# Kernel optimization log

Measured on AMD Instinct MI355X. Metric: run time of the kernel, lower is better.

Reference implementation:

```python
import math
import jax, jax.numpy as jnp
import numpy as np

C = 1.0          # Poincare ball curvature
NUM_HEADS = 8
EPS = 1e-15

def _beta(a, b):
    # Beta function via lgamma (python float constant)
    return math.exp(math.lgamma(a) + math.lgamma(b) - math.lgamma(a + b))

def h_linear(x, z, r, c=C):
    """HNN++ Poincare fully-connected layer (hypll HLinear).
    x: [..., in] points in the ball; z: [in, out] tangent weights; r: [out] bias."""
    sc = math.sqrt(c)
    x2 = jnp.sum(x * x, axis=-1, keepdims=True)
    lam = 2.0 / (1.0 - c * x2)                                # conformal factor
    zn = jnp.maximum(jnp.linalg.norm(z, axis=0), EPS)          # [out]
    inner = x @ z                                              # [..., out]
    two_scr = 2.0 * sc * r
    d = (2.0 * zn / sc) * jnp.arcsinh(
        (sc * inner * lam / zn) * jnp.cosh(two_scr) - (lam - 1.0) * jnp.sinh(two_scr)
    )
    w = jnp.sinh(sc * d) / sc
    return w / (1.0 + jnp.sqrt(1.0 + c * jnp.sum(w * w, axis=-1, keepdims=True)))

def pairwise_dist(q, k, c=C):
    """Poincare distance d(q,k) = arccosh(1 + 2c|q-k|^2 / ((1-c|q|^2)(1-c|k|^2))) / sqrt(c).
    q,k: [B,H,S,hd] -> [B,H,S,S]."""
    q2 = jnp.sum(q * q, axis=-1)
    k2 = jnp.sum(k * k, axis=-1)
    qk = jnp.einsum('bhqd,bhkd->bhqk', q, k)
    diff2 = jnp.maximum(q2[..., :, None] + k2[..., None, :] - 2.0 * qk, 0.0)
    denom = (1.0 - c * q2)[..., :, None] * (1.0 - c * k2)[..., None, :]
    arg = 1.0 + 2.0 * c * diff2 / denom
    return jnp.arccosh(jnp.maximum(arg, 1.0 + 1e-7)) / math.sqrt(c)

def midpoint(v, w, c=C):
    """Weighted Mobius gyromidpoint: m = 1/2 (x) (sum w*lam*x / sum w*(lam-1)).
    v: [B,H,Sk,hd], w: [B,H,Sq,Sk] -> [B,H,Sq,hd]."""
    v2 = jnp.sum(v * v, axis=-1)                      # [B,H,Sk]
    lam = 2.0 / (1.0 - c * v2)
    num = jnp.einsum('bhqk,bhkd->bhqd', w * lam[..., None, :], v)
    den = jnp.maximum(jnp.einsum('bhqk,bhk->bhq', w, lam - 1.0), EPS)[..., None]
    g = num / den                                     # gyromidpoint pre-scaling
    sc = math.sqrt(c)
    gn = jnp.maximum(jnp.linalg.norm(g, axis=-1, keepdims=True), EPS)
    t = jnp.tanh(0.5 * jnp.arctanh(jnp.clip(sc * gn, 0.0, 1.0 - 1e-7)))
    return (t / sc) * g / gn

def _forward(query, key, value, Wq, bq, Wk, bk, Wv, bv, scale_tau, scale_gamma):
    B, S, E = query.shape
    H = NUM_HEADS
    hd = E // H
    # hyperbolic q/k/v projections, then split into heads: [B,H,S,hd]
    q = h_linear(query, Wq, bq).reshape(B, S, H, hd).transpose(0, 2, 1, 3)
    k = h_linear(key, Wk, bk).reshape(B, S, H, hd).transpose(0, 2, 1, 3)
    v = h_linear(value, Wv, bv).reshape(B, S, H, hd).transpose(0, 2, 1, 3)
    # similarity = -dist/tau - gamma with tau = exp(-scale_tau)
    sim = -pairwise_dist(q, k) * jnp.exp(scale_tau[0]) - scale_gamma[0]
    causal = jnp.triu(jnp.ones((S, S), dtype=bool), k=1)
    sim = jnp.where(causal, -jnp.inf, sim)
    w = jnp.exp(sim)                                  # 'exp' attention activation
    agg = midpoint(v, w)                              # [B,H,S,hd]
    agg = agg.transpose(0, 2, 1, 3).reshape(B, S, E)
    # HNN++ beta-concatenation of the per-head ball points
    scale = _beta(E / 2.0, 0.5) / _beta(hd / 2.0, 0.5)
    return agg * scale

def setup_inputs() -> dict:
    root = jax.random.key(0)
    ks = jax.random.split(root, 8)
    B, S, E = 1, 2048, 512
    s = 0.02  # keep points well inside the unit ball
    return {
        'query': s * jax.random.normal(ks[0], (B, S, E), jnp.float32),
        'key':   s * jax.random.normal(ks[1], (B, S, E), jnp.float32),
        'value': s * jax.random.normal(ks[2], (B, S, E), jnp.float32),
        'Wq': s * jax.random.normal(ks[3], (E, E), jnp.float32),
        'Wk': s * jax.random.normal(ks[4], (E, E), jnp.float32),
        'Wv': s * jax.random.normal(ks[5], (E, E), jnp.float32),
        'bq': jnp.zeros((E,), jnp.float32),
        'bk': jnp.zeros((E,), jnp.float32),
        'bv': jnp.zeros((E,), jnp.float32),
        'scale_tau': jnp.zeros((1,), jnp.float32),
        'scale_gamma': jnp.zeros((1,), jnp.float32),
    }

def reference(query, key, value, Wq, Wk, Wv, bq, bk, bv, scale_tau, scale_gamma):
    return _forward(query, key, value, Wq, bq, Wk, bk, Wv, bv, scale_tau, scale_gamma)
```

## Files before the change

kernel.cpp:

```cpp
#include <hip/hip_runtime.h>
#include <cmath>

#define H 8
#define SEQ 2048
#define EDIM 512
#define HD 64
#define EPSF 1e-15f

typedef short bf16x8 __attribute__((ext_vector_type(8)));
typedef float f32x4 __attribute__((ext_vector_type(4)));

#define FLAG_OFF  0
#define ZN_OFF    16
#define X2S_OFF   (ZN_OFF + 3 * EDIM)
#define STATS_OFF (X2S_OFF + 3 * SEQ)
#define CQ_OFF    (STATS_OFF + 3 * H * SEQ)
#define IK_OFF    (CQ_OFF + H * SEQ)
#define U16_OFF   (IK_OFF + H * SEQ + 16)
#define WT_U16    0
#define XB_U16    (WT_U16 + 3 * EDIM * EDIM)
#define QKVB_U16  (XB_U16 + 3 * SEQ * EDIM)
#define VT_U16    (QKVB_U16 + 3 * SEQ * EDIM)
#define U16_TOTAL (VT_U16 + H * 80 * SEQ)
#define PART_OFF  (U16_OFF + (U16_TOTAL + 1) / 2 + 16)

__device__ __forceinline__ float bf2f(unsigned short u){
  union { unsigned int i; float f; } v; v.i = ((unsigned int)u) << 16; return v.f;
}
__device__ __forceinline__ unsigned short f2bf(float f){
  union { float f; unsigned int i; } v; v.f = f;
  unsigned int x = v.i;
  unsigned int r = (x + 0x7fffu + ((x >> 16) & 1u)) >> 16;
  return (unsigned short)r;
}

__global__ void probe_kernel(const unsigned short* __restrict__ q, int* __restrict__ flag){
  const int t = threadIdx.x;
  float mx = 0.f;
  #pragma unroll
  for (int j = 0; j < 4; ++j) mx = fmaxf(mx, fabsf(bf2f(q[t * 4 + j])));
  #pragma unroll
  for (int m = 32; m >= 1; m >>= 1) mx = fmaxf(mx, __shfl_xor(mx, m, 64));
  if (t == 0) *flag = (mx > 1000.f) ? 1 : 0;
}

__global__ __launch_bounds__(256) void wcvt_kernel(
    const void* __restrict__ Wq, const void* __restrict__ Wk, const void* __restrict__ Wv,
    const int* __restrict__ flag, unsigned short* __restrict__ WT, float* __restrict__ zn)
{
  const int p = blockIdx.y;
  const int bi = blockIdx.x >> 3, bo = blockIdx.x & 7;
  const void* W = (p == 0) ? Wq : ((p == 1) ? Wk : Wv);
  const int t = threadIdx.x;
  const int isf32 = *flag;
  __shared__ float tile[64][65];

  #pragma unroll
  for (int j = 0; j < 16; ++j){
    int idx = t + 256 * j;
    int il = idx >> 6, ol = idx & 63;
    float val;
    if (isf32) val = ((const float*)W)[(size_t)(bi * 64 + il) * EDIM + bo * 64 + ol];
    else       val = bf2f(((const unsigned short*)W)[(size_t)(bi * 64 + il) * EDIM + bo * 64 + ol]);
    tile[il][ol] = val;
  }
  __syncthreads();
  if (t < 64){
    float s = 0.f;
    #pragma unroll 8
    for (int i = 0; i < 64; ++i){ float v = tile[i][t]; s += v * v; }
    atomicAdd(&zn[p * EDIM + bo * 64 + t], s);
  }
  #pragma unroll
  for (int j = 0; j < 16; ++j){
    int idx = t + 256 * j;
    int ol = idx >> 6, il = idx & 63;
    WT[((size_t)p * EDIM + bo * 64 + ol) * EDIM + bi * 64 + il] = f2bf(tile[il][ol]);
  }
}

__global__ __launch_bounds__(256) void xcvt_kernel(
    const void* __restrict__ Xq, const void* __restrict__ Xk, const void* __restrict__ Xv,
    const int* __restrict__ flag, unsigned short* __restrict__ Xb, float* __restrict__ x2s)
{
  const int p = blockIdx.y;
  const void* X = (p == 0) ? Xq : ((p == 1) ? Xk : Xv);
  const int row = blockIdx.x * 8 + (threadIdx.x >> 5);
  const int l = threadIdx.x & 31;
  const int isf32 = *flag;
  float s = 0.f;
  #pragma unroll
  for (int j = 0; j < 16; ++j){
    int i = l + 32 * j;
    float val;
    if (isf32) val = ((const float*)X)[(size_t)row * EDIM + i];
    else       val = bf2f(((const unsigned short*)X)[(size_t)row * EDIM + i]);
    Xb[((size_t)p * SEQ + row) * EDIM + i] = f2bf(val);
    s += val * val;
  }
  #pragma unroll
  for (int m = 16; m >= 1; m >>= 1) s += __shfl_xor(s, m, 64);
  if (l == 0) x2s[p * SEQ + row] = s;
}

__global__ __launch_bounds__(256) void hlinear_kernel(
    const unsigned short* __restrict__ Xb, const unsigned short* __restrict__ WT,
    const void* __restrict__ Bq, const void* __restrict__ Bk, const void* __restrict__ Bv,
    const float* __restrict__ znacc, const float* __restrict__ x2s_g,
    const int* __restrict__ flag,
    unsigned short* __restrict__ qkvb, float* __restrict__ stats,
    float* __restrict__ cqs, float* __restrict__ iks,
    unsigned short* __restrict__ VT)
{
  const int p = blockIdx.y;
  const void* Bb = (p == 0) ? Bq : ((p == 1) ? Bk : Bv);
  const int r0 = blockIdx.x * 8;
  const int t  = threadIdx.x;
  const int w = t >> 6, lane = t & 63;
  const int col = lane & 15, quad = lane >> 4;
  const int isf32 = *flag;

  __shared__ float smem[8 * EDIM];
  __shared__ float sw2[8];

  const unsigned short* Xrow = Xb + ((size_t)p * SEQ + r0 + (col & 7)) * EDIM;
  const unsigned short* WTb  = WT + ((size_t)p * EDIM + w * 128 + col) * EDIM;

  f32x4 acc[8];
  #pragma unroll
  for (int nt = 0; nt < 8; ++nt) acc[nt] = (f32x4){0.f, 0.f, 0.f, 0.f};

  for (int ks = 0; ks < 16; ++ks){
    bf16x8 af = *(const bf16x8*)&Xrow[ks * 32 + quad * 8];
    #pragma unroll
    for (int nt = 0; nt < 8; ++nt){
      bf16x8 bf = *(const bf16x8*)&WTb[(size_t)nt * 16 * EDIM + ks * 32 + quad * 8];
      acc[nt] = __builtin_amdgcn_mfma_f32_16x16x32_bf16(af, bf, acc[nt], 0, 0, 0);
    }
  }

  if (quad < 2){
    float lamr[4], lm1[4];
    #pragma unroll
    for (int r = 0; r < 4; ++r){
      float x2 = x2s_g[p * SEQ + r0 + quad * 4 + r];
      lamr[r] = 2.f / (1.f - x2);
      lm1[r] = lamr[r] - 1.f;
    }
    #pragma unroll
    for (int nt = 0; nt < 8; ++nt){
      const int n = w * 128 + nt * 16 + col;
      float znv = fmaxf(sqrtf(znacc[p * EDIM + n]), EPSF);
      float rb;
      if (isf32) rb = ((const float*)Bb)[n];
      else       rb = bf2f(((const unsigned short*)Bb)[n]);
      float e2r = __expf(2.f * rb);
      float ie2r = 1.f / e2r;
      float ch = 0.5f * (e2r + ie2r), sh = 0.5f * (e2r - ie2r);
      float izn = 1.f / znv;
      float tz = 2.f * znv;
      #pragma unroll
      for (int r = 0; r < 4; ++r){
        float a = (acc[nt][r] * lamr[r] * izn) * ch - lm1[r] * sh;
        float b = a + sqrtf(a * a + 1.f);
        float tt = __expf(tz * __logf(b));
        smem[(quad * 4 + r) * EDIM + n] = 0.5f * (tt - 1.f / tt);
      }
    }
  }
  __syncthreads();

  {
    int row = t >> 5, l = t & 31;
    float s = 0.f;
    for (int o = l; o < EDIM; o += 32){ float wv = smem[row * EDIM + o]; s += wv * wv; }
    #pragma unroll
    for (int m = 16; m >= 1; m >>= 1) s += __shfl_xor(s, m, 64);
    if (l == 0) sw2[row] = s;
  }
  __syncthreads();

  const int o0 = 2 * t;
  const int h0 = t >> 5;
  const int d0 = o0 & 63;
  #pragma unroll
  for (int rr = 0; rr < 8; ++rr){
    float inv = 1.f / (1.f + sqrtf(1.f + sw2[rr]));
    unsigned short b0 = f2bf(smem[rr * EDIM + o0] * inv);
    unsigned short b1 = f2bf(smem[rr * EDIM + o0 + 1] * inv);
    float r0v = bf2f(b0), r1v = bf2f(b1);
    int s = r0 + rr;
    unsigned int* dst = (unsigned int*)&qkvb[(((size_t)p * H + h0) * SEQ + s) * HD + d0];
    *dst = (unsigned int)b0 | ((unsigned int)b1 << 16);
    float ss = r0v * r0v + r1v * r1v;
    #pragma unroll
    for (int m = 16; m >= 1; m >>= 1) ss += __shfl_xor(ss, m, 64);
    if (p == 2){
      float lam = 2.f / (1.f - ss);
      VT[((size_t)h0 * 80 + d0) * SEQ + s]     = f2bf(r0v * lam);
      VT[((size_t)h0 * 80 + d0 + 1) * SEQ + s] = f2bf(r1v * lam);
      if ((t & 31) == 0) VT[((size_t)h0 * 80 + 64) * SEQ + s] = f2bf(lam - 1.f);
    }
    if ((t & 31) == 0){
      stats[((size_t)p * H + h0) * SEQ + s] = ss;
      if (p == 0) cqs[(size_t)h0 * SEQ + s] = 2.f / (1.f - ss);
      if (p == 1) iks[(size_t)h0 * SEQ + s] = 1.f / (1.f - ss);
    }
  }
}

__global__ __launch_bounds__(256) void attn_part_kernel(
    const unsigned short* __restrict__ Qb, const unsigned short* __restrict__ Kb,
    const unsigned short* __restrict__ VT,
    const float* __restrict__ q2s_all, const float* __restrict__ k2s_all,
    const float* __restrict__ cqs_all, const float* __restrict__ iks_all,
    const void* __restrict__ tau, const void* __restrict__ gam,
    const int* __restrict__ flag, float4* __restrict__ part)
{
  const int h  = blockIdx.y;
  const int tile = blockIdx.x >> 1;
  const int sl = blockIdx.x & 1;
  const int t = threadIdx.x;
  const int w = t >> 6, lane = t & 63;
  const int col = lane & 15, quad = lane >> 4;
  const int q0 = tile * 16;

  const unsigned short* Qh  = Qb + (size_t)h * SEQ * HD;
  const unsigned short* Kh  = Kb + (size_t)h * SEQ * HD;
  const unsigned short* VTh = VT + (size_t)h * 80 * SEQ;
  const float* q2s = q2s_all + (size_t)h * SEQ;
  const float* k2s = k2s_all + (size_t)h * SEQ;
  const float* cqs = cqs_all + (size_t)h * SEQ;
  const float* iks = iks_all + (size_t)h * SEQ;

  __shared__ float red[4][64][20];

  float tauv, gamv;
  if (*flag){ tauv = ((const float*)tau)[0]; gamv = ((const float*)gam)[0]; }
  else      { tauv = bf2f(((const unsigned short*)tau)[0]);
              gamv = bf2f(((const unsigned short*)gam)[0]); }
  const float e_tau = expf(tauv);

  const int srcA = ((quad & 1) * 2) * 16 + col;
  const int srcB = srcA + 16;
  const int tsel = quad >> 1;

  bf16x8 qf0 = *(const bf16x8*)&Qh[(size_t)(q0 + col) * HD + quad * 8];
  bf16x8 qf1 = *(const bf16x8*)&Qh[(size_t)(q0 + col) * HD + 32 + quad * 8];
  const float q2 = q2s[q0 + col];
  const float cq = cqs[q0 + col];
  const int qmax = q0 + col;

  f32x4 pv[5];
  #pragma unroll
  for (int nt = 0; nt < 5; ++nt) pv[nt] = (f32x4){0.f, 0.f, 0.f, 0.f};

  const int nch = (tile + 4) >> 2;
  for (int kc = sl * 4 + w; kc < nch; kc += 8){
    #pragma unroll
    for (int half = 0; half < 2; ++half){
      const int kb32 = kc * 64 + half * 32;
      unsigned int tlo[2], thi[2];
      #pragma unroll
      for (int tt = 0; tt < 2; ++tt){
        const int kbase = kb32 + 16 * tt;
        bf16x8 kf0 = *(const bf16x8*)&Kh[(size_t)(kbase + col) * HD + quad * 8];
        bf16x8 kf1 = *(const bf16x8*)&Kh[(size_t)(kbase + col) * HD + 32 + quad * 8];
        f32x4 s = (f32x4){0.f, 0.f, 0.f, 0.f};
        s = __builtin_amdgcn_mfma_f32_16x16x32_bf16(kf0, qf0, s, 0, 0, 0);
        s = __builtin_amdgcn_mfma_f32_16x16x32_bf16(kf1, qf1, s, 0, 0, 0);
        float4 k2q = *(const float4*)&k2s[kbase + quad * 4];
        float4 ikq = *(const float4*)&iks[kbase + quad * 4];
        unsigned short pb[4];
        #pragma unroll
        for (int r = 0; r < 4; ++r){
          float k2 = (r == 0) ? k2q.x : (r == 1) ? k2q.y : (r == 2) ? k2q.z : k2q.w;
          float ik = (r == 0) ? ikq.x : (r == 1) ? ikq.y : (r == 2) ? ikq.z : ikq.w;
          float diff2 = fmaxf(q2 + k2 - 2.f * s[r], 0.f);
          float u = diff2 * cq * ik;
          u = fmaxf(u, 1e-7f);
          float z = 1.f + u + sqrtf(u * (u + 2.f));
          float wv = __expf(-e_tau * __logf(z) - gamv);
          int key = kbase + quad * 4 + r;
          if (key > qmax) wv = 0.f;
          pb[r] = f2bf(wv);
        }
        tlo[tt] = (unsigned int)pb[0] | ((unsigned int)pb[1] << 16);
        thi[tt] = (unsigned int)pb[2] | ((unsigned int)pb[3] << 16);
      }
      unsigned int a0 = (unsigned int)__shfl((int)tlo[0], srcA, 64);
      unsigned int a1 = (unsigned int)__shfl((int)tlo[1], srcA, 64);
      unsigned int b0 = (unsigned int)__shfl((int)thi[0], srcA, 64);
      unsigned int b1 = (unsigned int)__shfl((int)thi[1], srcA, 64);
      unsigned int c0 = (unsigned int)__shfl((int)tlo[0], srcB, 64);
      unsigned int c1 = (unsigned int)__shfl((int)tlo[1], srcB, 64);
      unsigned int d0 = (unsigned int)__shfl((int)thi[0], srcB, 64);
      unsigned int d1 = (unsigned int)__shfl((int)thi[1], srcB, 64);
      union { uint4 u; bf16x8 v; } pw;
      pw.u.x = tsel ? a1 : a0;
      pw.u.y = tsel ? b1 : b0;
      pw.u.z = tsel ? c1 : c0;
      pw.u.w = tsel ? d1 : d0;
      #pragma unroll
      for (int nt = 0; nt < 5; ++nt){
        bf16x8 vf = *(const bf16x8*)&VTh[(size_t)(16 * nt + col) * SEQ + kb32 + quad * 8];
        pv[nt] = __builtin_amdgcn_mfma_f32_16x16x32_bf16(pw.v, vf, pv[nt], 0, 0, 0);
      }
    }
  }

  #pragma unroll
  for (int nt = 0; nt < 5; ++nt)
    *(float4*)&red[w][lane][nt * 4] = (float4){pv[nt][0], pv[nt][1], pv[nt][2], pv[nt][3]};
  __syncthreads();

  if (t < 64){
    const size_t base = (((size_t)h * 128 + tile) * 2 + sl) * 5;
    #pragma unroll
    for (int nt = 0; nt < 5; ++nt){
      float4 a = *(const float4*)&red[0][t][nt * 4];
      float4 b = *(const float4*)&red[1][t][nt * 4];
      float4 c = *(const float4*)&red[2][t][nt * 4];
      float4 d = *(const float4*)&red[3][t][nt * 4];
      part[(base + nt) * 64 + t] =
          (float4){a.x + b.x + c.x + d.x, a.y + b.y + c.y + d.y,
                   a.z + b.z + c.z + d.z, a.w + b.w + c.w + d.w};
    }
  }
}

__global__ __launch_bounds__(64) void attn_fin_kernel(
    const float4* __restrict__ part, float* __restrict__ out, float beta_scale)
{
  const int h = blockIdx.y, tile = blockIdx.x;
  const int t = threadIdx.x;
  const int col = t & 15, quad = t >> 4;
  const int q0 = tile * 16;

  f32x4 pv[5];
  const size_t b0 = (((size_t)h * 128 + tile) * 2 + 0) * 5;
  const size_t b1 = (((size_t)h * 128 + tile) * 2 + 1) * 5;
  #pragma unroll
  for (int nt = 0; nt < 5; ++nt){
    float4 a = part[(b0 + nt) * 64 + t];
    float4 b = part[(b1 + nt) * 64 + t];
    pv[nt] = (f32x4){a.x + b.x, a.y + b.y, a.z + b.z, a.w + b.w};
  }

  #pragma unroll
  for (int r = 0; r < 4; ++r){
    float den = __shfl(pv[4][r], quad * 16, 64);
    den = fmaxf(den, EPSF);
    float inv_den = 1.f / den;
    float g[4];
    float gsq = 0.f;
    #pragma unroll
    for (int nt = 0; nt < 4; ++nt){ g[nt] = pv[nt][r] * inv_den; gsq += g[nt] * g[nt]; }
    #pragma unroll
    for (int m = 8; m >= 1; m >>= 1) gsq += __shfl_xor(gsq, m, 64);
    float gn = fmaxf(sqrtf(gsq), EPSF);
    float x = fminf(gn, 1.f - 1e-7f);
    float tt2 = x / (1.f + sqrtf(1.f - x * x));
    float scl = (tt2 / gn) * beta_scale;
    const int q = q0 + quad * 4 + r;
    #pragma unroll
    for (int nt = 0; nt < 4; ++nt)
      out[(size_t)q * EDIM + h * HD + 16 * nt + col] = g[nt] * scl;
  }
}

extern "C" void kernel_launch(void* const* d_in, const int* in_sizes, int n_in,
                              void* d_out, int out_size, void* d_ws, size_t ws_size,
                              hipStream_t stream){
  const void* Xq  = d_in[0];
  const void* Xk  = d_in[1];
  const void* Xv  = d_in[2];
  const void* Wq  = d_in[3];
  const void* Wk  = d_in[4];
  const void* Wv  = d_in[5];
  const void* Bq  = d_in[6];
  const void* Bk  = d_in[7];
  const void* Bv  = d_in[8];
  const void* tau = d_in[9];
  const void* gam = d_in[10];

  float* wsf   = (float*)d_ws;
  int*   flag  = (int*)(wsf + FLAG_OFF);
  float* zn    = wsf + ZN_OFF;
  float* x2s   = wsf + X2S_OFF;
  float* stats = wsf + STATS_OFF;
  float* cqs   = wsf + CQ_OFF;
  float* iks   = wsf + IK_OFF;
  unsigned short* u16b = (unsigned short*)(wsf + U16_OFF);
  unsigned short* WT   = u16b + WT_U16;
  unsigned short* Xb   = u16b + XB_U16;
  unsigned short* qkvb = u16b + QKVB_U16;
  unsigned short* VT   = u16b + VT_U16;
  float4* part = (float4*)(wsf + PART_OFF);

  unsigned short* Qb = qkvb;
  unsigned short* Kb = qkvb + (size_t)H * SEQ * HD;
  float* q2s = stats;
  float* k2s = stats + (size_t)H * SEQ;

  double lb1 = lgamma(EDIM / 2.0) + lgamma(0.5) - lgamma(EDIM / 2.0 + 0.5);
  double lb2 = lgamma(HD / 2.0)   + lgamma(0.5) - lgamma(HD / 2.0 + 0.5);
  float beta_scale = (float)exp(lb1 - lb2);

  probe_kernel<<<dim3(1), dim3(64), 0, stream>>>((const unsigned short*)Xq, flag);
  hipMemsetAsync(zn, 0, 3 * EDIM * sizeof(float), stream);
  hipMemsetAsync(VT, 0, (size_t)H * 80 * SEQ * sizeof(unsigned short), stream);
  wcvt_kernel<<<dim3(64, 3), dim3(256), 0, stream>>>(Wq, Wk, Wv, flag, WT, zn);
  xcvt_kernel<<<dim3(SEQ / 8, 3), dim3(256), 0, stream>>>(Xq, Xk, Xv, flag, Xb, x2s);
  hlinear_kernel<<<dim3(SEQ / 8, 3), dim3(256), 0, stream>>>(
      Xb, WT, Bq, Bk, Bv, zn, x2s, flag, qkvb, stats, cqs, iks, VT);
  attn_part_kernel<<<dim3(256, H), dim3(256), 0, stream>>>(
      Qb, Kb, VT, q2s, k2s, cqs, iks, tau, gam, flag, part);
  attn_fin_kernel<<<dim3(128, H), dim3(64), 0, stream>>>(
      part, (float*)d_out, beta_scale);
}
```

Measured before the change: 231.6 us.

## Fuse input conversion into HLinear and use atomic split-K attention accumulation

Removes the separate input-conversion kernel: the HLinear GEMM now reads raw inputs, converts them to bf16 and computes row norms in-register, and handles 16 rows per block so no MFMA rows are wasted. The attention kernel is restructured so each block covers 64 queries (one per wave) and splits the causal key chunks across 8 slices, with early exit for empty slices. Partial results go into a zeroed fp32 accumulator through atomics, replacing the shared-memory reduction and partial buffer. In exchange it adds atomic traffic, a larger memset, and a summation order that is no longer deterministic.

```diff
diff --git a/kernel.cpp b/kernel.cpp
--- a/kernel.cpp
+++ b/kernel.cpp
@@ -12,17 +12,14 @@
 
 #define FLAG_OFF  0
 #define ZN_OFF    16
-#define X2S_OFF   (ZN_OFF + 3 * EDIM)
-#define STATS_OFF (X2S_OFF + 3 * SEQ)
+#define ACC_OFF   (ZN_OFF + 3 * EDIM)
+#define STATS_OFF (ACC_OFF + H * SEQ * 80)
 #define CQ_OFF    (STATS_OFF + 3 * H * SEQ)
 #define IK_OFF    (CQ_OFF + H * SEQ)
 #define U16_OFF   (IK_OFF + H * SEQ + 16)
 #define WT_U16    0
-#define XB_U16    (WT_U16 + 3 * EDIM * EDIM)
-#define QKVB_U16  (XB_U16 + 3 * SEQ * EDIM)
+#define QKVB_U16  (WT_U16 + 3 * EDIM * EDIM)
 #define VT_U16    (QKVB_U16 + 3 * SEQ * EDIM)
-#define U16_TOTAL (VT_U16 + H * 80 * SEQ)
-#define PART_OFF  (U16_OFF + (U16_TOTAL + 1) / 2 + 16)
 
 __device__ __forceinline__ float bf2f(unsigned short u){
   union { unsigned int i; float f; } v; v.i = ((unsigned int)u) << 16; return v.f;
@@ -79,103 +76,92 @@
   }
 }
 
-__global__ __launch_bounds__(256) void xcvt_kernel(
+__global__ __launch_bounds__(256) void hlinear_kernel(
     const void* __restrict__ Xq, const void* __restrict__ Xk, const void* __restrict__ Xv,
-    const int* __restrict__ flag, unsigned short* __restrict__ Xb, float* __restrict__ x2s)
-{
-  const int p = blockIdx.y;
-  const void* X = (p == 0) ? Xq : ((p == 1) ? Xk : Xv);
-  const int row = blockIdx.x * 8 + (threadIdx.x >> 5);
-  const int l = threadIdx.x & 31;
-  const int isf32 = *flag;
-  float s = 0.f;
-  #pragma unroll
-  for (int j = 0; j < 16; ++j){
-    int i = l + 32 * j;
-    float val;
-    if (isf32) val = ((const float*)X)[(size_t)row * EDIM + i];
-    else       val = bf2f(((const unsigned short*)X)[(size_t)row * EDIM + i]);
-    Xb[((size_t)p * SEQ + row) * EDIM + i] = f2bf(val);
-    s += val * val;
-  }
-  #pragma unroll
-  for (int m = 16; m >= 1; m >>= 1) s += __shfl_xor(s, m, 64);
-  if (l == 0) x2s[p * SEQ + row] = s;
-}
-
-__global__ __launch_bounds__(256) void hlinear_kernel(
-    const unsigned short* __restrict__ Xb, const unsigned short* __restrict__ WT,
+    const unsigned short* __restrict__ WT,
     const void* __restrict__ Bq, const void* __restrict__ Bk, const void* __restrict__ Bv,
-    const float* __restrict__ znacc, const float* __restrict__ x2s_g,
-    const int* __restrict__ flag,
+    const float* __restrict__ znacc, const int* __restrict__ flag,
     unsigned short* __restrict__ qkvb, float* __restrict__ stats,
     float* __restrict__ cqs, float* __restrict__ iks,
     unsigned short* __restrict__ VT)
 {
   const int p = blockIdx.y;
+  const void* X  = (p == 0) ? Xq : ((p == 1) ? Xk : Xv);
   const void* Bb = (p == 0) ? Bq : ((p == 1) ? Bk : Bv);
-  const int r0 = blockIdx.x * 8;
+  const int r0 = blockIdx.x * 16;
   const int t  = threadIdx.x;
   const int w = t >> 6, lane = t & 63;
   const int col = lane & 15, quad = lane >> 4;
   const int isf32 = *flag;
 
-  __shared__ float smem[8 * EDIM];
-  __shared__ float sw2[8];
-
-  const unsigned short* Xrow = Xb + ((size_t)p * SEQ + r0 + (col & 7)) * EDIM;
-  const unsigned short* WTb  = WT + ((size_t)p * EDIM + w * 128 + col) * EDIM;
+  __shared__ float smem[16 * EDIM];
+  __shared__ float sw2[16];
+
+  const unsigned short* WTb = WT + ((size_t)p * EDIM + w * 128 + col) * EDIM;
+  const float* Xf = (const float*)X + (size_t)(r0 + col) * EDIM;
+  const unsigned short* Xh = (const unsigned short*)X + (size_t)(r0 + col) * EDIM;
 
   f32x4 acc[8];
   #pragma unroll
   for (int nt = 0; nt < 8; ++nt) acc[nt] = (f32x4){0.f, 0.f, 0.f, 0.f};
+  float x2part = 0.f;
 
   for (int ks = 0; ks < 16; ++ks){
-    bf16x8 af = *(const bf16x8*)&Xrow[ks * 32 + quad * 8];
+    bf16x8 af;
+    if (isf32){
+      float4 xa = *(const float4*)&Xf[ks * 32 + quad * 8];
+      float4 xb = *(const float4*)&Xf[ks * 32 + quad * 8 + 4];
+      float xv[8] = {xa.x, xa.y, xa.z, xa.w, xb.x, xb.y, xb.z, xb.w};
+      #pragma unroll
+      for (int j = 0; j < 8; ++j){ af[j] = (short)f2bf(xv[j]); x2part += xv[j] * xv[j]; }
+    } else {
+      af = *(const bf16x8*)&Xh[ks * 32 + quad * 8];
+      #pragma unroll
+      for (int j = 0; j < 8; ++j){ float xv = bf2f((unsigned short)af[j]); x2part += xv * xv; }
+    }
     #pragma unroll
     for (int nt = 0; nt < 8; ++nt){
       bf16x8 bf = *(const bf16x8*)&WTb[(size_t)nt * 16 * EDIM + ks * 32 + quad * 8];
       acc[nt] = __builtin_amdgcn_mfma_f32_16x16x32_bf16(af, bf, acc[nt], 0, 0, 0);
     }
   }
-
-  if (quad < 2){
-    float lamr[4], lm1[4];
+  x2part += __shfl_xor(x2part, 16, 64);
+  x2part += __shfl_xor(x2part, 32, 64);
+  float lamr[4], lm1[4];
+  #pragma unroll
+  for (int r = 0; r < 4; ++r){
+    float x2r = __shfl(x2part, quad * 4 + r, 64);
+    lamr[r] = 2.f / (1.f - x2r);
+    lm1[r] = lamr[r] - 1.f;
+  }
+  #pragma unroll
+  for (int nt = 0; nt < 8; ++nt){
+    const int n = w * 128 + nt * 16 + col;
+    float znv = fmaxf(sqrtf(znacc[p * EDIM + n]), EPSF);
+    float rb;
+    if (isf32) rb = ((const float*)Bb)[n];
+    else       rb = bf2f(((const unsigned short*)Bb)[n]);
+    float e2r = __expf(2.f * rb);
+    float ie2r = 1.f / e2r;
+    float ch = 0.5f * (e2r + ie2r), sh = 0.5f * (e2r - ie2r);
+    float izn = 1.f / znv;
+    float tz = 2.f * znv;
     #pragma unroll
     for (int r = 0; r < 4; ++r){
-      float x2 = x2s_g[p * SEQ + r0 + quad * 4 + r];
-      lamr[r] = 2.f / (1.f - x2);
-      lm1[r] = lamr[r] - 1.f;
-    }
-    #pragma unroll
-    for (int nt = 0; nt < 8; ++nt){
-      const int n = w * 128 + nt * 16 + col;
-      float znv = fmaxf(sqrtf(znacc[p * EDIM + n]), EPSF);
-      float rb;
-      if (isf32) rb = ((const float*)Bb)[n];
-      else       rb = bf2f(((const unsigned short*)Bb)[n]);
-      float e2r = __expf(2.f * rb);
-      float ie2r = 1.f / e2r;
-      float ch = 0.5f * (e2r + ie2r), sh = 0.5f * (e2r - ie2r);
-      float izn = 1.f / znv;
-      float tz = 2.f * znv;
-      #pragma unroll
-      for (int r = 0; r < 4; ++r){
-        float a = (acc[nt][r] * lamr[r] * izn) * ch - lm1[r] * sh;
-        float b = a + sqrtf(a * a + 1.f);
-        float tt = __expf(tz * __logf(b));
-        smem[(quad * 4 + r) * EDIM + n] = 0.5f * (tt - 1.f / tt);
-      }
+      float a = (acc[nt][r] * lamr[r] * izn) * ch - lm1[r] * sh;
+      float b = a + sqrtf(a * a + 1.f);
+      float tt = __expf(tz * __logf(b));
+      smem[(quad * 4 + r) * EDIM + n] = 0.5f * (tt - 1.f / tt);
     }
   }
   __syncthreads();
 
   {
-    int row = t >> 5, l = t & 31;
+    int row = t >> 4, l = t & 15;
     float s = 0.f;
-    for (int o = l; o < EDIM; o += 32){ float wv = smem[row * EDIM + o]; s += wv * wv; }
-    #pragma unroll
-    for (int m = 16; m >= 1; m >>= 1) s += __shfl_xor(s, m, 64);
+    for (int o = l; o < EDIM; o += 16){ float wv = smem[row * EDIM + o]; s += wv * wv; }
+    #pragma unroll
+    for (int m = 8; m >= 1; m >>= 1) s += __shfl_xor(s, m, 16);
     if (l == 0) sw2[row] = s;
   }
   __syncthreads();
@@ -183,8 +169,9 @@
   const int o0 = 2 * t;
   const int h0 = t >> 5;
   const int d0 = o0 & 63;
-  #pragma unroll
-  for (int rr = 0; rr < 8; ++rr){
+  const int l5 = t & 31;
+  #pragma unroll
+  for (int rr = 0; rr < 16; ++rr){
     float inv = 1.f / (1.f + sqrtf(1.f + sw2[rr]));
     unsigned short b0 = f2bf(smem[rr * EDIM + o0] * inv);
     unsigned short b1 = f2bf(smem[rr * EDIM + o0 + 1] * inv);
@@ -199,9 +186,10 @@
       float lam = 2.f / (1.f - ss);
       VT[((size_t)h0 * 80 + d0) * SEQ + s]     = f2bf(r0v * lam);
       VT[((size_t)h0 * 80 + d0 + 1) * SEQ + s] = f2bf(r1v * lam);
-      if ((t & 31) == 0) VT[((size_t)h0 * 80 + 64) * SEQ + s] = f2bf(lam - 1.f);
-    }
-    if ((t & 31) == 0){
+      if (l5 < 16)
+        VT[((size_t)h0 * 80 + 64 + l5) * SEQ + s] = (l5 == 0) ? f2bf(lam - 1.f) : 0;
+    }
+    if (l5 == 0){
       stats[((size_t)p * H + h0) * SEQ + s] = ss;
       if (p == 0) cqs[(size_t)h0 * SEQ + s] = 2.f / (1.f - ss);
       if (p == 1) iks[(size_t)h0 * SEQ + s] = 1.f / (1.f - ss);
@@ -209,21 +197,22 @@
   }
 }
 
-__global__ __launch_bounds__(256) void attn_part_kernel(
+__global__ __launch_bounds__(256) void attn_kernel(
     const unsigned short* __restrict__ Qb, const unsigned short* __restrict__ Kb,
     const unsigned short* __restrict__ VT,
     const float* __restrict__ q2s_all, const float* __restrict__ k2s_all,
     const float* __restrict__ cqs_all, const float* __restrict__ iks_all,
     const void* __restrict__ tau, const void* __restrict__ gam,
-    const int* __restrict__ flag, float4* __restrict__ part)
+    const int* __restrict__ flag, float* __restrict__ ACC)
 {
   const int h  = blockIdx.y;
-  const int tile = blockIdx.x >> 1;
-  const int sl = blockIdx.x & 1;
+  const int tile = blockIdx.x >> 3;
+  const int sl = blockIdx.x & 7;
+  if (sl > tile) return;
   const int t = threadIdx.x;
   const int w = t >> 6, lane = t & 63;
   const int col = lane & 15, quad = lane >> 4;
-  const int q0 = tile * 16;
+  const int q0 = tile * 64 + w * 16;
 
   const unsigned short* Qh  = Qb + (size_t)h * SEQ * HD;
   const unsigned short* Kh  = Kb + (size_t)h * SEQ * HD;
@@ -233,8 +222,6 @@
   const float* cqs = cqs_all + (size_t)h * SEQ;
   const float* iks = iks_all + (size_t)h * SEQ;
 
-  __shared__ float red[4][64][20];
-
   float tauv, gamv;
   if (*flag){ tauv = ((const float*)tau)[0]; gamv = ((const float*)gam)[0]; }
   else      { tauv = bf2f(((const unsigned short*)tau)[0]);
@@ -255,8 +242,7 @@
   #pragma unroll
   for (int nt = 0; nt < 5; ++nt) pv[nt] = (f32x4){0.f, 0.f, 0.f, 0.f};
 
-  const int nch = (tile + 4) >> 2;
-  for (int kc = sl * 4 + w; kc < nch; kc += 8){
+  for (int kc = sl; kc <= tile; kc += 8){
     #pragma unroll
     for (int half = 0; half < 2; ++half){
       const int kb32 = kc * 64 + half * 32;
@@ -277,8 +263,7 @@
           float k2 = (r == 0) ? k2q.x : (r == 1) ? k2q.y : (r == 2) ? k2q.z : k2q.w;
           float ik = (r == 0) ? ikq.x : (r == 1) ? ikq.y : (r == 2) ? ikq.z : ikq.w;
           float diff2 = fmaxf(q2 + k2 - 2.f * s[r], 0.f);
-          float u = diff2 * cq * ik;
-          u = fmaxf(u, 1e-7f);
+          float u = fmaxf(diff2 * cq * ik, 1e-7f);
           float z = 1.f + u + sqrtf(u * (u + 2.f));
           float wv = __expf(-e_tau * __logf(z) - gamv);
           int key = kbase + quad * 4 + r;
@@ -310,27 +295,16 @@
   }
 
   #pragma unroll
-  for (int nt = 0; nt < 5; ++nt)
-    *(float4*)&red[w][lane][nt * 4] = (float4){pv[nt][0], pv[nt][1], pv[nt][2], pv[nt][3]};
-  __syncthreads();
-
-  if (t < 64){
-    const size_t base = (((size_t)h * 128 + tile) * 2 + sl) * 5;
-    #pragma unroll
-    for (int nt = 0; nt < 5; ++nt){
-      float4 a = *(const float4*)&red[0][t][nt * 4];
-      float4 b = *(const float4*)&red[1][t][nt * 4];
-      float4 c = *(const float4*)&red[2][t][nt * 4];
-      float4 d = *(const float4*)&red[3][t][nt * 4];
-      part[(base + nt) * 64 + t] =
-          (float4){a.x + b.x + c.x + d.x, a.y + b.y + c.y + d.y,
-                   a.z + b.z + c.z + d.z, a.w + b.w + c.w + d.w};
-    }
+  for (int r = 0; r < 4; ++r){
+    float* row = ACC + ((size_t)h * SEQ + q0 + quad * 4 + r) * 80;
+    #pragma unroll
+    for (int nt = 0; nt < 5; ++nt)
+      atomicAdd(&row[16 * nt + col], pv[nt][r]);
   }
 }
 
 __global__ __launch_bounds__(64) void attn_fin_kernel(
-    const float4* __restrict__ part, float* __restrict__ out, float beta_scale)
+    const float* __restrict__ ACC, float* __restrict__ out, float beta_scale)
 {
   const int h = blockIdx.y, tile = blockIdx.x;
   const int t = threadIdx.x;
@@ -338,14 +312,11 @@
   const int q0 = tile * 16;
 
   f32x4 pv[5];
-  const size_t b0 = (((size_t)h * 128 + tile) * 2 + 0) * 5;
-  const size_t b1 = (((size_t)h * 128 + tile) * 2 + 1) * 5;
-  #pragma unroll
-  for (int nt = 0; nt < 5; ++nt){
-    float4 a = part[(b0 + nt) * 64 + t];
-    float4 b = part[(b1 + nt) * 64 + t];
-    pv[nt] = (f32x4){a.x + b.x, a.y + b.y, a.z + b.z, a.w + b.w};
-  }
+  #pragma unroll
+  for (int nt = 0; nt < 5; ++nt)
+    #pragma unroll
+    for (int r = 0; r < 4; ++r)
+      pv[nt][r] = ACC[((size_t)h * SEQ + q0 + quad * 4 + r) * 80 + 16 * nt + col];
 
   #pragma unroll
   for (int r = 0; r < 4; ++r){
@@ -387,16 +358,14 @@
   float* wsf   = (float*)d_ws;
   int*   flag  = (int*)(wsf + FLAG_OFF);
   float* zn    = wsf + ZN_OFF;
-  float* x2s   = wsf + X2S_OFF;
+  float* ACC   = wsf + ACC_OFF;
   float* stats = wsf + STATS_OFF;
   float* cqs   = wsf + CQ_OFF;
   float* iks   = wsf + IK_OFF;
   unsigned short* u16b = (unsigned short*)(wsf + U16_OFF);
   unsigned short* WT   = u16b + WT_U16;
-  unsigned short* Xb   = u16b + XB_U16;
   unsigned short* qkvb = u16b + QKVB_U16;
   unsigned short* VT   = u16b + VT_U16;
-  float4* part = (float4*)(wsf + PART_OFF);
 
   unsigned short* Qb = qkvb;
   unsigned short* Kb = qkvb + (size_t)H * SEQ * HD;
@@ -408,14 +377,12 @@
   float beta_scale = (float)exp(lb1 - lb2);
 
   probe_kernel<<<dim3(1), dim3(64), 0, stream>>>((const unsigned short*)Xq, flag);
-  hipMemsetAsync(zn, 0, 3 * EDIM * sizeof(float), stream);
-  hipMemsetAsync(VT, 0, (size_t)H * 80 * SEQ * sizeof(unsigned short), stream);
+  hipMemsetAsync(zn, 0, (size_t)(3 * EDIM + H * SEQ * 80) * sizeof(float), stream);
   wcvt_kernel<<<dim3(64, 3), dim3(256), 0, stream>>>(Wq, Wk, Wv, flag, WT, zn);
-  xcvt_kernel<<<dim3(SEQ / 8, 3), dim3(256), 0, stream>>>(Xq, Xk, Xv, flag, Xb, x2s);
-  hlinear_kernel<<<dim3(SEQ / 8, 3), dim3(256), 0, stream>>>(
-      Xb, WT, Bq, Bk, Bv, zn, x2s, flag, qkvb, stats, cqs, iks, VT);
-  attn_part_kernel<<<dim3(256, H), dim3(256), 0, stream>>>(
-      Qb, Kb, VT, q2s, k2s, cqs, iks, tau, gam, flag, part);
+  hlinear_kernel<<<dim3(SEQ / 16, 3), dim3(256), 0, stream>>>(
+      Xq, Xk, Xv, WT, Bq, Bk, Bv, zn, flag, qkvb, stats, cqs, iks, VT);
+  attn_kernel<<<dim3(32 * 8, H), dim3(256), 0, stream>>>(
+      Qb, Kb, VT, q2s, k2s, cqs, iks, tau, gam, flag, ACC);
   attn_fin_kernel<<<dim3(128, H), dim3(64), 0, stream>>>(
-      part, (float*)d_out, beta_scale);
-}
+      ACC, (float*)d_out, beta_scale);
+}
```

Result: faster. 219.0 us (-5.4%).
